# Kernel tuning notes

Measured on AMD Instinct MI355X. Metric: run time of the kernel, lower is better.

The kernel has to match this reference:

```python
import jax, jax.numpy as jnp
import numpy as np

B, C, T = 128, 16, 2048
H = 256            # hidden_size
G = 4 * H          # gate dim (i, f, g, o in torch order)
NUM_OUT = 10


def setup_inputs() -> dict:
    key = jax.random.key(0)
    ks = jax.random.split(key, 7)
    s = 1.0 / np.sqrt(H)  # torch default LSTM init scale
    return {
        "x": jax.random.normal(ks[0], (B, C, T), dtype=jnp.float32),
        "w_ih": jax.random.uniform(ks[1], (G, C), minval=-s, maxval=s, dtype=jnp.float32),
        "w_hh": jax.random.uniform(ks[2], (G, H), minval=-s, maxval=s, dtype=jnp.float32),
        "b_ih": jax.random.uniform(ks[3], (G,), minval=-s, maxval=s, dtype=jnp.float32),
        "b_hh": jax.random.uniform(ks[4], (G,), minval=-s, maxval=s, dtype=jnp.float32),
        "w_out": jax.random.uniform(ks[5], (NUM_OUT, H), minval=-s, maxval=s, dtype=jnp.float32),
        "b_out": jax.random.uniform(ks[6], (NUM_OUT,), minval=-s, maxval=s, dtype=jnp.float32),
    }


def _lstm_last_hidden(x, w_ih, w_hh, b_ih, b_hh):
    # x: (B, C, T) -> (B, T, C)
    xt = jnp.swapaxes(x, 1, 2)
    # Precompute input projections for all timesteps: (B, T, 4H)
    xproj = jnp.einsum('btc,gc->btg', xt, w_ih) + b_ih + b_hh
    xs = jnp.swapaxes(xproj, 0, 1)  # (T, B, 4H) for scan

    h0 = jnp.zeros((xt.shape[0], w_hh.shape[1]), dtype=x.dtype)
    c0 = jnp.zeros_like(h0)

    def step(carry, xp):
        h, cell = carry
        gates = xp + h @ w_hh.T               # (B, 4H)
        i, f, g, o = jnp.split(gates, 4, axis=-1)  # torch gate order i,f,g,o
        i = jax.nn.sigmoid(i)
        f = jax.nn.sigmoid(f)
        g = jnp.tanh(g)
        o = jax.nn.sigmoid(o)
        cell = f * cell + i * g
        h = o * jnp.tanh(cell)
        return (h, cell), None

    (hT, _), _ = jax.lax.scan(step, (h0, c0), xs)
    return hT  # (B, H): hidden state at last timestep


def reference(x, w_ih, w_hh, b_ih, b_hh, w_out, b_out):
    # bn0 is Identity (c.normalize_data=True)
    hT = _lstm_last_hidden(x, w_ih, w_hh, b_ih, b_hh)
    logits = hT @ w_out.T + b_out  # (B, num_outputs)
    return jax.nn.log_softmax(logits, axis=1)
```

## Files before the change

kernel.cpp:

```cpp
#include <hip/hip_runtime.h>
#include <cstdint>
#include <cstddef>

#define NB 128
#define NC 16
#define NT 2048
#define NH 256
#define NG 1024
#define NO 10

typedef _Float16 f16;
typedef _Float16 h2 __attribute__((ext_vector_type(2)));
typedef _Float16 h8 __attribute__((ext_vector_type(8)));

#define HPHASE 544

static __device__ __forceinline__ float fdot2(h2 a, h2 b, float c) {
#if __has_builtin(__builtin_amdgcn_fdot2)
  return __builtin_amdgcn_fdot2(a, b, c, false);
#else
  return c + (float)a[0] * (float)b[0] + (float)a[1] * (float)b[1];
#endif
}

static __device__ __forceinline__ int sdot4(int a, int b, int c) {
#if __has_builtin(__builtin_amdgcn_sdot4)
  return __builtin_amdgcn_sdot4(a, b, c, false);
#else
  int r = c;
#pragma unroll
  for (int i = 0; i < 4; ++i)
    r += (int)(int8_t)(a >> (8 * i)) * (int)(int8_t)(b >> (8 * i));
  return r;
#endif
}

static __device__ __forceinline__ float pairswap(float v) {
  int r = __builtin_amdgcn_update_dpp(0, __builtin_bit_cast(int, v),
                                      0xB1, 0xF, 0xF, true);
  return __builtin_bit_cast(float, r);
}

static __device__ __forceinline__ float sigm(float x) {
  return __builtin_amdgcn_rcpf(1.f + __expf(-x));
}
static __device__ __forceinline__ float tanh_(float x) {
  return 1.f - 2.f * __builtin_amdgcn_rcpf(1.f + __expf(2.f * x));
}

__global__ void prepack_whh_i8(const float* __restrict__ whh,
                               int8_t* __restrict__ wq,
                               float* __restrict__ scale) {
  int row = blockIdx.x;
  int k   = threadIdx.x;
  float v = whh[row * NH + k];
  float m = fabsf(v);
  for (int off = 32; off; off >>= 1) m = fmaxf(m, __shfl_xor(m, off, 64));
  __shared__ float smax[4];
  if ((k & 63) == 0) smax[k >> 6] = m;
  __syncthreads();
  float mm = fmaxf(fmaxf(smax[0], smax[1]), fmaxf(smax[2], smax[3]));
  float s = fmaxf(mm, 1e-20f) / 127.f;
  int qv = (int)rintf(v / s);
  qv = min(127, max(-127, qv));
  wq[row * NH + k] = (int8_t)qv;
  if (k == 0) scale[row] = s;
}

__global__ __launch_bounds__(512, 1)
void lstm_main(const float* __restrict__ x,
               const float* __restrict__ w_ih,
               const float* __restrict__ b_ih,
               const float* __restrict__ b_hh,
               const float* __restrict__ w_out,
               const float* __restrict__ b_out,
               const int8_t* __restrict__ wq,
               const float* __restrict__ scales,
               float* __restrict__ out) {
  const int t = threadIdx.x;
  const int u = t >> 1;
  const int half = t & 1;
  const int b = blockIdx.x;

  __shared__ __align__(16) int8_t hq8[2 * HPHASE];
  __shared__ __align__(16) f16 xs[64][NC];
  __shared__ float hT[NH];
  __shared__ float lg[NO];

  int wi_[32], wf_[32], wg_[32], wo_[32];
  h2 wih[4][4];
  {
    const int4* pi = (const int4*)(wq + (size_t)u * NH + 128 * half);
    const int4* pf = (const int4*)(wq + (size_t)(256 + u) * NH + 128 * half);
    const int4* pg = (const int4*)(wq + (size_t)(512 + u) * NH + 128 * half);
    const int4* po = (const int4*)(wq + (size_t)(768 + u) * NH + 128 * half);
#pragma unroll
    for (int c = 0; c < 8; ++c) {
      int4 vi = pi[c], vf = pf[c], vg = pg[c], vo = po[c];
      wi_[4 * c + 0] = vi.x; wi_[4 * c + 1] = vi.y; wi_[4 * c + 2] = vi.z; wi_[4 * c + 3] = vi.w;
      wf_[4 * c + 0] = vf.x; wf_[4 * c + 1] = vf.y; wf_[4 * c + 2] = vf.z; wf_[4 * c + 3] = vf.w;
      wg_[4 * c + 0] = vg.x; wg_[4 * c + 1] = vg.y; wg_[4 * c + 2] = vg.z; wg_[4 * c + 3] = vg.w;
      wo_[4 * c + 0] = vo.x; wo_[4 * c + 1] = vo.y; wo_[4 * c + 2] = vo.z; wo_[4 * c + 3] = vo.w;
    }
  }
#pragma unroll
  for (int g4 = 0; g4 < 4; ++g4) {
    int row = u + 256 * g4;
#pragma unroll
    for (int uu = 0; uu < 4; ++uu) {
      h2 t2 = {(f16)w_ih[row * NC + 8 * half + 2 * uu],
               (f16)w_ih[row * NC + 8 * half + 2 * uu + 1]};
      wih[g4][uu] = t2;
    }
  }
  const float K = 1.f / 127.f;
  float sci = scales[u] * K;
  float scf = scales[256 + u] * K;
  float scg = scales[512 + u] * K;
  float sco = scales[768 + u] * K;
  float bi_ = half ? 0.f : b_ih[u] + b_hh[u];
  float bf_ = half ? 0.f : b_ih[256 + u] + b_hh[256 + u];
  float bg_ = half ? 0.f : b_ih[512 + u] + b_hh[512 + u];
  float bo_ = half ? 0.f : b_ih[768 + u] + b_hh[768 + u];

  for (int e = t; e < 2 * HPHASE; e += 512) hq8[e] = 0;
#pragma unroll
  for (int r = 0; r < 2; ++r) {
    int e = t + 512 * r;
    int cc = e >> 6, tt = e & 63;
    xs[tt][cc] = (f16)x[(size_t)(b * NC + cc) * NT + tt];
  }
  __syncthreads();

  float c_ = 0.f, h_last = 0.f;
  const int rdoff = 400 * half;
  const int wroff = 272 * half + u;

#pragma unroll 1
  for (int s = 0; s < NT; ++s) {
    const int p = s & 1;
    const int4* hrd = (const int4*)(hq8 + p * HPHASE + rdoff);

    float fi = bi_, ff = bf_, fg_ = bg_, fo = bo_;
    {
      h8 xv = *(const h8*)&xs[s & 63][8 * half];
#pragma unroll
      for (int uu = 0; uu < 4; ++uu) {
        h2 xp = {xv[2 * uu], xv[2 * uu + 1]};
        fi = fdot2(xp, wih[0][uu], fi);
        ff = fdot2(xp, wih[1][uu], ff);
        fg_ = fdot2(xp, wih[2][uu], fg_);
        fo = fdot2(xp, wih[3][uu], fo);
      }
    }

    int ai = 0, af = 0, ag = 0, ao = 0;
#pragma unroll
    for (int c = 0; c < 8; ++c) {
      int4 hv = hrd[c];
      ai = sdot4(hv.x, wi_[4 * c + 0], ai); ai = sdot4(hv.y, wi_[4 * c + 1], ai);
      ai = sdot4(hv.z, wi_[4 * c + 2], ai); ai = sdot4(hv.w, wi_[4 * c + 3], ai);
      af = sdot4(hv.x, wf_[4 * c + 0], af); af = sdot4(hv.y, wf_[4 * c + 1], af);
      af = sdot4(hv.z, wf_[4 * c + 2], af); af = sdot4(hv.w, wf_[4 * c + 3], af);
      ag = sdot4(hv.x, wg_[4 * c + 0], ag); ag = sdot4(hv.y, wg_[4 * c + 1], ag);
      ag = sdot4(hv.z, wg_[4 * c + 2], ag); ag = sdot4(hv.w, wg_[4 * c + 3], ag);
      ao = sdot4(hv.x, wo_[4 * c + 0], ao); ao = sdot4(hv.y, wo_[4 * c + 1], ao);
      ao = sdot4(hv.z, wo_[4 * c + 2], ao); ao = sdot4(hv.w, wo_[4 * c + 3], ao);
    }

    float vi = fi + (float)ai * sci;
    float vf = ff + (float)af * scf;
    float vg = fg_ + (float)ag * scg;
    float vo = fo + (float)ao * sco;
    vi += pairswap(vi); vf += pairswap(vf); vg += pairswap(vg); vo += pairswap(vo);

    float ig = sigm(vi);
    float fgate = sigm(vf);
    float gv = tanh_(vg);
    float og = sigm(vo);
    c_ = fgate * c_ + ig * gv;
    float hh = og * tanh_(c_);
    h_last = hh;
    hq8[(1 - p) * HPHASE + wroff] = (int8_t)(int)rintf(hh * 127.f);

    if ((s & 63) == 63 && s != NT - 1) {
      __syncthreads();
#pragma unroll
      for (int r = 0; r < 2; ++r) {
        int e = t + 512 * r;
        int cc = e >> 6, tt = e & 63;
        xs[tt][cc] = (f16)x[(size_t)(b * NC + cc) * NT + (s + 1) + tt];
      }
    }
    __syncthreads();
  }

  if (!half) hT[u] = h_last;
  __syncthreads();
  if (t < NO) {
    float acc = b_out[t];
    for (int k = 0; k < NH; ++k) acc += hT[k] * w_out[t * NH + k];
    lg[t] = acc;
  }
  __syncthreads();
  if (t == 0) {
    float m = lg[0];
    for (int o = 1; o < NO; ++o) m = fmaxf(m, lg[o]);
    float ssum = 0.f;
    for (int o = 0; o < NO; ++o) ssum += __expf(lg[o] - m);
    float lse = m + __logf(ssum);
    for (int o = 0; o < NO; ++o) out[b * NO + o] = lg[o] - lse;
  }
}

extern "C" void kernel_launch(void* const* d_in, const int* in_sizes, int n_in,
                              void* d_out, int out_size, void* d_ws, size_t ws_size,
                              hipStream_t stream) {
  const float* x    = (const float*)d_in[0];
  const float* wih  = (const float*)d_in[1];
  const float* whh  = (const float*)d_in[2];
  const float* bih  = (const float*)d_in[3];
  const float* bhh  = (const float*)d_in[4];
  const float* wout = (const float*)d_in[5];
  const float* bout = (const float*)d_in[6];
  float* out = (float*)d_out;
  int8_t* wq = (int8_t*)d_ws;
  float* scales = (float*)((char*)d_ws + NG * NH);

  hipLaunchKernelGGL(prepack_whh_i8, dim3(NG), dim3(NH), 0, stream, whh, wq, scales);
  hipLaunchKernelGGL(lstm_main, dim3(NB), dim3(512), 0, stream,
                     x, wih, bih, bhh, wout, bout, wq, scales, out);
}
```

Measured before the change: 1.810 ms.

## Preload full input sequence into LDS and software-pipeline input projection

Stages the entire 2048-step input for the batch row into shared memory (64 KB of f16) once at kernel start, which removes the periodic block-wide refill and its extra barrier every 64 steps. The input-projection dot products for step s+1 are computed after the h write of step s, before the barrier, so they sit off the critical path of the next step's recurrent matmul. The trade-off is a much larger LDS footprint and a longer serial prologue load. It also carries four extra live registers across iterations.

```diff
diff --git a/kernel.cpp b/kernel.cpp
--- a/kernel.cpp
+++ b/kernel.cpp
@@ -82,8 +82,8 @@
   const int half = t & 1;
   const int b = blockIdx.x;
 
+  __shared__ __align__(16) f16 xs[NT][NC];
   __shared__ __align__(16) int8_t hq8[2 * HPHASE];
-  __shared__ __align__(16) f16 xs[64][NC];
   __shared__ float hT[NH];
   __shared__ float lg[NO];
 
@@ -124,10 +124,10 @@
   float bo_ = half ? 0.f : b_ih[768 + u] + b_hh[768 + u];
 
   for (int e = t; e < 2 * HPHASE; e += 512) hq8[e] = 0;
-#pragma unroll
-  for (int r = 0; r < 2; ++r) {
+#pragma unroll 1
+  for (int r = 0; r < 64; ++r) {
     int e = t + 512 * r;
-    int cc = e >> 6, tt = e & 63;
+    int cc = e >> 11, tt = e & 2047;
     xs[tt][cc] = (f16)x[(size_t)(b * NC + cc) * NT + tt];
   }
   __syncthreads();
@@ -135,24 +135,24 @@
   float c_ = 0.f, h_last = 0.f;
   const int rdoff = 400 * half;
   const int wroff = 272 * half + u;
+
+  float xai = bi_, xaf = bf_, xag = bg_, xao = bo_;
+  {
+    h8 xv = *(const h8*)&xs[0][8 * half];
+#pragma unroll
+    for (int uu = 0; uu < 4; ++uu) {
+      h2 xp = {xv[2 * uu], xv[2 * uu + 1]};
+      xai = fdot2(xp, wih[0][uu], xai);
+      xaf = fdot2(xp, wih[1][uu], xaf);
+      xag = fdot2(xp, wih[2][uu], xag);
+      xao = fdot2(xp, wih[3][uu], xao);
+    }
+  }
 
 #pragma unroll 1
   for (int s = 0; s < NT; ++s) {
     const int p = s & 1;
     const int4* hrd = (const int4*)(hq8 + p * HPHASE + rdoff);
-
-    float fi = bi_, ff = bf_, fg_ = bg_, fo = bo_;
-    {
-      h8 xv = *(const h8*)&xs[s & 63][8 * half];
-#pragma unroll
-      for (int uu = 0; uu < 4; ++uu) {
-        h2 xp = {xv[2 * uu], xv[2 * uu + 1]};
-        fi = fdot2(xp, wih[0][uu], fi);
-        ff = fdot2(xp, wih[1][uu], ff);
-        fg_ = fdot2(xp, wih[2][uu], fg_);
-        fo = fdot2(xp, wih[3][uu], fo);
-      }
-    }
 
     int ai = 0, af = 0, ag = 0, ao = 0;
 #pragma unroll
@@ -168,10 +168,10 @@
       ao = sdot4(hv.z, wo_[4 * c + 2], ao); ao = sdot4(hv.w, wo_[4 * c + 3], ao);
     }
 
-    float vi = fi + (float)ai * sci;
-    float vf = ff + (float)af * scf;
-    float vg = fg_ + (float)ag * scg;
-    float vo = fo + (float)ao * sco;
+    float vi = xai + (float)ai * sci;
+    float vf = xaf + (float)af * scf;
+    float vg = xag + (float)ag * scg;
+    float vo = xao + (float)ao * sco;
     vi += pairswap(vi); vf += pairswap(vf); vg += pairswap(vg); vo += pairswap(vo);
 
     float ig = sigm(vi);
@@ -183,15 +183,21 @@
     h_last = hh;
     hq8[(1 - p) * HPHASE + wroff] = (int8_t)(int)rintf(hh * 127.f);
 
-    if ((s & 63) == 63 && s != NT - 1) {
-      __syncthreads();
-#pragma unroll
-      for (int r = 0; r < 2; ++r) {
-        int e = t + 512 * r;
-        int cc = e >> 6, tt = e & 63;
-        xs[tt][cc] = (f16)x[(size_t)(b * NC + cc) * NT + (s + 1) + tt];
+    {
+      int sn = (s + 1) & (NT - 1);
+      h8 xv = *(const h8*)&xs[sn][8 * half];
+      float ni = bi_, nf = bf_, ng = bg_, no_ = bo_;
+#pragma unroll
+      for (int uu = 0; uu < 4; ++uu) {
+        h2 xp = {xv[2 * uu], xv[2 * uu + 1]};
+        ni = fdot2(xp, wih[0][uu], ni);
+        nf = fdot2(xp, wih[1][uu], nf);
+        ng = fdot2(xp, wih[2][uu], ng);
+        no_ = fdot2(xp, wih[3][uu], no_);
       }
-    }
+      xai = ni; xaf = nf; xag = ng; xao = no_;
+    }
+
     __syncthreads();
   }
 
```

Result: slower. 1.853 ms (+2.4%).

## Split LSTM gates across thread pairs instead of splitting the hidden dimension

Applied to the files above, without the earlier changes.

Each thread pair now partitions the four gates (one thread does i and g, the other f and o) over the full hidden vector, instead of both threads computing all four gates over half of K. This removes the four per-step DPP pair reductions, leaving two pairswaps that exchange finished activations, and each thread evaluates two transcendentals instead of four, with tanh expressed through sigmoid. The padded shared layout is dropped: every thread reads the whole h vector (16 int4 loads) from a plain [2][256] buffer and only the even thread writes h. The cost is twice the LDS read volume per thread, possible bank conflicts or broadcast reads, and the same 128 weight registers per thread.

```diff
diff --git a/kernel.cpp b/kernel.cpp
--- a/kernel.cpp
+++ b/kernel.cpp
@@ -13,8 +13,6 @@
 typedef _Float16 h2 __attribute__((ext_vector_type(2)));
 typedef _Float16 h8 __attribute__((ext_vector_type(8)));
 
-#define HPHASE 544
-
 static __device__ __forceinline__ float fdot2(h2 a, h2 b, float c) {
 #if __has_builtin(__builtin_amdgcn_fdot2)
   return __builtin_amdgcn_fdot2(a, b, c, false);
@@ -43,9 +41,6 @@
 
 static __device__ __forceinline__ float sigm(float x) {
   return __builtin_amdgcn_rcpf(1.f + __expf(-x));
-}
-static __device__ __forceinline__ float tanh_(float x) {
-  return 1.f - 2.f * __builtin_amdgcn_rcpf(1.f + __expf(2.f * x));
 }
 
 __global__ void prepack_whh_i8(const float* __restrict__ whh,
@@ -82,48 +77,43 @@
   const int half = t & 1;
   const int b = blockIdx.x;
 
-  __shared__ __align__(16) int8_t hq8[2 * HPHASE];
+  __shared__ __align__(16) int8_t hq8[2][NH];
   __shared__ __align__(16) f16 xs[64][NC];
   __shared__ float hT[NH];
   __shared__ float lg[NO];
 
-  int wi_[32], wf_[32], wg_[32], wo_[32];
-  h2 wih[4][4];
+  const int rowA = (half ? 256 : 0) + u;
+  const int rowB = (half ? 768 : 512) + u;
+
+  int wa_[64], wb_[64];
+  h2 wihA[8], wihB[8];
   {
-    const int4* pi = (const int4*)(wq + (size_t)u * NH + 128 * half);
-    const int4* pf = (const int4*)(wq + (size_t)(256 + u) * NH + 128 * half);
-    const int4* pg = (const int4*)(wq + (size_t)(512 + u) * NH + 128 * half);
-    const int4* po = (const int4*)(wq + (size_t)(768 + u) * NH + 128 * half);
-#pragma unroll
-    for (int c = 0; c < 8; ++c) {
-      int4 vi = pi[c], vf = pf[c], vg = pg[c], vo = po[c];
-      wi_[4 * c + 0] = vi.x; wi_[4 * c + 1] = vi.y; wi_[4 * c + 2] = vi.z; wi_[4 * c + 3] = vi.w;
-      wf_[4 * c + 0] = vf.x; wf_[4 * c + 1] = vf.y; wf_[4 * c + 2] = vf.z; wf_[4 * c + 3] = vf.w;
-      wg_[4 * c + 0] = vg.x; wg_[4 * c + 1] = vg.y; wg_[4 * c + 2] = vg.z; wg_[4 * c + 3] = vg.w;
-      wo_[4 * c + 0] = vo.x; wo_[4 * c + 1] = vo.y; wo_[4 * c + 2] = vo.z; wo_[4 * c + 3] = vo.w;
-    }
-  }
-#pragma unroll
-  for (int g4 = 0; g4 < 4; ++g4) {
-    int row = u + 256 * g4;
-#pragma unroll
-    for (int uu = 0; uu < 4; ++uu) {
-      h2 t2 = {(f16)w_ih[row * NC + 8 * half + 2 * uu],
-               (f16)w_ih[row * NC + 8 * half + 2 * uu + 1]};
-      wih[g4][uu] = t2;
-    }
+    const int4* pa = (const int4*)(wq + (size_t)rowA * NH);
+    const int4* pb = (const int4*)(wq + (size_t)rowB * NH);
+#pragma unroll
+    for (int c = 0; c < 16; ++c) {
+      int4 va = pa[c], vb = pb[c];
+      wa_[4 * c + 0] = va.x; wa_[4 * c + 1] = va.y; wa_[4 * c + 2] = va.z; wa_[4 * c + 3] = va.w;
+      wb_[4 * c + 0] = vb.x; wb_[4 * c + 1] = vb.y; wb_[4 * c + 2] = vb.z; wb_[4 * c + 3] = vb.w;
+    }
+  }
+#pragma unroll
+  for (int uu = 0; uu < 8; ++uu) {
+    h2 ta = {(f16)w_ih[rowA * NC + 2 * uu], (f16)w_ih[rowA * NC + 2 * uu + 1]};
+    h2 tb = {(f16)w_ih[rowB * NC + 2 * uu], (f16)w_ih[rowB * NC + 2 * uu + 1]};
+    wihA[uu] = ta;
+    wihB[uu] = tb;
   }
   const float K = 1.f / 127.f;
-  float sci = scales[u] * K;
-  float scf = scales[256 + u] * K;
-  float scg = scales[512 + u] * K;
-  float sco = scales[768 + u] * K;
-  float bi_ = half ? 0.f : b_ih[u] + b_hh[u];
-  float bf_ = half ? 0.f : b_ih[256 + u] + b_hh[256 + u];
-  float bg_ = half ? 0.f : b_ih[512 + u] + b_hh[512 + u];
-  float bo_ = half ? 0.f : b_ih[768 + u] + b_hh[768 + u];
-
-  for (int e = t; e < 2 * HPHASE; e += 512) hq8[e] = 0;
+  const float scA = scales[rowA] * K;
+  const float scB = scales[rowB] * K;
+  const float bA = b_ih[rowA] + b_hh[rowA];
+  const float bB = b_ih[rowB] + b_hh[rowB];
+
+  if (t < 2 * NH) hq8[0][t] = 0;
+  {
+    int cc = t >> 6, tt = t & 63;
+  }
 #pragma unroll
   for (int r = 0; r < 2; ++r) {
     int e = t + 512 * r;
@@ -133,55 +123,62 @@
   __syncthreads();
 
   float c_ = 0.f, h_last = 0.f;
-  const int rdoff = 400 * half;
-  const int wroff = 272 * half + u;
 
 #pragma unroll 1
   for (int s = 0; s < NT; ++s) {
     const int p = s & 1;
-    const int4* hrd = (const int4*)(hq8 + p * HPHASE + rdoff);
-
-    float fi = bi_, ff = bf_, fg_ = bg_, fo = bo_;
+    const int4* hrd = (const int4*)&hq8[p][0];
+
+    float xa = bA, xb = bB;
     {
-      h8 xv = *(const h8*)&xs[s & 63][8 * half];
+      const h8* xr = (const h8*)&xs[s & 63][0];
+      h8 x0 = xr[0], x1 = xr[1];
 #pragma unroll
       for (int uu = 0; uu < 4; ++uu) {
-        h2 xp = {xv[2 * uu], xv[2 * uu + 1]};
-        fi = fdot2(xp, wih[0][uu], fi);
-        ff = fdot2(xp, wih[1][uu], ff);
-        fg_ = fdot2(xp, wih[2][uu], fg_);
-        fo = fdot2(xp, wih[3][uu], fo);
+        h2 xp0 = {x0[2 * uu], x0[2 * uu + 1]};
+        h2 xp1 = {x1[2 * uu], x1[2 * uu + 1]};
+        xa = fdot2(xp0, wihA[uu], xa);
+        xa = fdot2(xp1, wihA[uu + 4], xa);
+        xb = fdot2(xp0, wihB[uu], xb);
+        xb = fdot2(xp1, wihB[uu + 4], xb);
       }
     }
 
-    int ai = 0, af = 0, ag = 0, ao = 0;
+    int a0 = 0, a0b = 0, b0 = 0, b0b = 0;
 #pragma unroll
     for (int c = 0; c < 8; ++c) {
-      int4 hv = hrd[c];
-      ai = sdot4(hv.x, wi_[4 * c + 0], ai); ai = sdot4(hv.y, wi_[4 * c + 1], ai);
-      ai = sdot4(hv.z, wi_[4 * c + 2], ai); ai = sdot4(hv.w, wi_[4 * c + 3], ai);
-      af = sdot4(hv.x, wf_[4 * c + 0], af); af = sdot4(hv.y, wf_[4 * c + 1], af);
-      af = sdot4(hv.z, wf_[4 * c + 2], af); af = sdot4(hv.w, wf_[4 * c + 3], af);
-      ag = sdot4(hv.x, wg_[4 * c + 0], ag); ag = sdot4(hv.y, wg_[4 * c + 1], ag);
-      ag = sdot4(hv.z, wg_[4 * c + 2], ag); ag = sdot4(hv.w, wg_[4 * c + 3], ag);
-      ao = sdot4(hv.x, wo_[4 * c + 0], ao); ao = sdot4(hv.y, wo_[4 * c + 1], ao);
-      ao = sdot4(hv.z, wo_[4 * c + 2], ao); ao = sdot4(hv.w, wo_[4 * c + 3], ao);
-    }
-
-    float vi = fi + (float)ai * sci;
-    float vf = ff + (float)af * scf;
-    float vg = fg_ + (float)ag * scg;
-    float vo = fo + (float)ao * sco;
-    vi += pairswap(vi); vf += pairswap(vf); vg += pairswap(vg); vo += pairswap(vo);
-
-    float ig = sigm(vi);
-    float fgate = sigm(vf);
-    float gv = tanh_(vg);
-    float og = sigm(vo);
-    c_ = fgate * c_ + ig * gv;
-    float hh = og * tanh_(c_);
+      int4 h0 = hrd[2 * c];
+      int4 h1 = hrd[2 * c + 1];
+      a0 = sdot4(h0.x, wa_[8 * c + 0], a0); a0 = sdot4(h0.y, wa_[8 * c + 1], a0);
+      a0 = sdot4(h0.z, wa_[8 * c + 2], a0); a0 = sdot4(h0.w, wa_[8 * c + 3], a0);
+      a0b = sdot4(h1.x, wa_[8 * c + 4], a0b); a0b = sdot4(h1.y, wa_[8 * c + 5], a0b);
+      a0b = sdot4(h1.z, wa_[8 * c + 6], a0b); a0b = sdot4(h1.w, wa_[8 * c + 7], a0b);
+      b0 = sdot4(h0.x, wb_[8 * c + 0], b0); b0 = sdot4(h0.y, wb_[8 * c + 1], b0);
+      b0 = sdot4(h0.z, wb_[8 * c + 2], b0); b0 = sdot4(h0.w, wb_[8 * c + 3], b0);
+      b0b = sdot4(h1.x, wb_[8 * c + 4], b0b); b0b = sdot4(h1.y, wb_[8 * c + 5], b0b);
+      b0b = sdot4(h1.z, wb_[8 * c + 6], b0b); b0b = sdot4(h1.w, wb_[8 * c + 7], b0b);
+    }
+
+    float va = xa + (float)(a0 + a0b) * scA;
+    float vb = xb + (float)(b0 + b0b) * scB;
+
+    float ta = sigm(va);
+    float argb = half ? vb : 2.f * vb;
+    float sb = sigm(argb);
+    float tb = half ? sb : 2.f * sb - 1.f;
+
+    float ea = pairswap(ta);
+    float eb = pairswap(tb);
+    float ig = half ? ea : ta;
+    float fg = half ? ta : ea;
+    float gv = half ? eb : tb;
+    float og = half ? tb : eb;
+
+    c_ = fg * c_ + ig * gv;
+    float tc = sigm(2.f * c_);
+    float hh = og * (2.f * tc - 1.f);
     h_last = hh;
-    hq8[(1 - p) * HPHASE + wroff] = (int8_t)(int)rintf(hh * 127.f);
+    if (!half) hq8[1 - p][u] = (int8_t)(int)rintf(hh * 127.f);
 
     if ((s & 63) == 63 && s != NT - 1) {
       __syncthreads();
```

Measured after the change: 1.936 ms. +7.0%, slower.
